# Kernel optimization log

Measured on AMD Instinct MI355X. Metric: run time of the kernel, lower is better.

The kernel has to match this reference:

```python
import jax, jax.numpy as jnp
import numpy as np

HIDDEN_DIM = 1024
N_EXPERTS = 4
EPS = 1e-6


def rmsnorm(x, w):
    return x * jax.lax.rsqrt(jnp.mean(x * x, axis=-1, keepdims=True) + EPS) * w


def setup_inputs() -> dict:
    key = jax.random.key(0)
    k1, k2, k3 = jax.random.split(key, 3)
    B, S = 16, 4096
    x = jax.random.normal(k1, (B, S, HIDDEN_DIM), dtype=jnp.float32)
    experts = jax.random.randint(k2, (B,), 0, N_EXPERTS)
    norm1_w = jnp.ones((HIDDEN_DIM,), dtype=jnp.float32)
    norm2_w = jnp.ones((HIDDEN_DIM,), dtype=jnp.float32)
    time_decay_logit = jnp.full((HIDDEN_DIM,), 2.0, dtype=jnp.float32)
    # stacked expert weights [n_experts, out, in] (torch Linear stores [out, in])
    W_experts = jax.random.normal(k3, (N_EXPERTS, HIDDEN_DIM, HIDDEN_DIM), dtype=jnp.float32) * 0.02
    return {"x": x, "experts": experts, "norm1_w": norm1_w,
            "time_decay_logit": time_decay_logit, "norm2_w": norm2_w,
            "W_experts": W_experts}


def reference(x, experts, norm1_w, time_decay_logit, norm2_w, W_experts):
    B, S, D = x.shape
    x_norm = rmsnorm(x, norm1_w)                      # [B,S,D]
    decay = jax.nn.sigmoid(time_decay_logit)          # [D]

    def step(state, x_t):
        state = state * decay + x_t * (1.0 - decay)
        return state, state

    init = jnp.zeros((B, D), dtype=x.dtype)
    _, states = jax.lax.scan(step, init, jnp.swapaxes(x_norm, 0, 1))  # [S,B,D]
    x = x + jnp.swapaxes(states, 0, 1)                # residual add

    pool_state = rmsnorm(x, norm2_w)[:, -1, :]        # [B,D]
    # gather each sample's expert weight and apply: y = relu(x @ W^T)
    W_b = W_experts[experts]                          # [B,out,in]
    out = jax.nn.relu(jnp.einsum('bd,bod->bo', pool_state, W_b))
    return out
```

## Files before the change

### kernel.cpp

```cpp
#include <hip/hip_runtime.h>
#include <math.h>

#define EPS 1e-6f
#define CH_L 64
#define TG 16

__global__ void k_prep(const float* __restrict__ logit, float* __restrict__ decay,
                       float* __restrict__ coef, int* __restrict__ Kp, int D, int S) {
    int tid = threadIdx.x;
    float local = 0.f;
    for (int d = tid; d < D; d += blockDim.x) {
        float dec = 1.f / (1.f + expf(-logit[d]));
        decay[d] = dec;
        coef[d]  = 1.f - dec;
        local = fmaxf(local, dec);
    }
    for (int off = 32; off; off >>= 1) local = fmaxf(local, __shfl_down(local, off));
    __shared__ float red[4];
    int wv = tid >> 6, ln = tid & 63;
    if (ln == 0) red[wv] = local;
    __syncthreads();
    if (tid == 0) {
        float maxd = fmaxf(fmaxf(red[0], red[1]), fmaxf(red[2], red[3]));
        float Kf;
        if (maxd <= 0.f) {
            Kf = 1.f;
        } else {
            float lg = logf(maxd);
            if (lg >= 0.f) Kf = (float)S;
            else           Kf = logf(1e-12f) / lg;
        }
        int K = (Kf >= (float)S) ? S : ((int)Kf + 1);
        *Kp = K;
    }
}

__global__ void k_rms(const float4* __restrict__ x4, const int* __restrict__ Kp,
                      float* __restrict__ inv_rms, int B, int S, int D, int nchunk) {
    int tg = blockIdx.x, b = blockIdx.y;
    int K = *Kp;
    int cmax = K / CH_L; if (cmax > nchunk - 1) cmax = nchunk - 1;
    int maxdist = (cmax + 1) * CH_L;
    int t0 = tg * TG;
    if (S - (t0 + TG) >= maxdist) return;
    int tid = threadIdx.x;
    int d4 = D >> 2;
    float s[TG];
#pragma unroll
    for (int i = 0; i < TG; i++) {
        float4 v = x4[((size_t)(b * S + t0 + i)) * d4 + tid];
        s[i] = v.x * v.x + v.y * v.y + v.z * v.z + v.w * v.w;
    }
#pragma unroll
    for (int i = 0; i < TG; i++)
        for (int off = 32; off; off >>= 1) s[i] += __shfl_down(s[i], off);
    __shared__ float red[4][TG];
    int wv = tid >> 6, ln = tid & 63;
    if (ln == 0) {
#pragma unroll
        for (int i = 0; i < TG; i++) red[wv][i] = s[i];
    }
    __syncthreads();
    if (tid < TG) {
        float tot = red[0][tid] + red[1][tid] + red[2][tid] + red[3][tid];
        inv_rms[(size_t)b * S + t0 + tid] = rsqrtf(tot / (float)D + EPS);
    }
}

__global__ void k_ema(const float4* __restrict__ x4, const float* __restrict__ inv_rms,
                      const float4* __restrict__ decay4, const float4* __restrict__ coef4,
                      const float4* __restrict__ w14, const int* __restrict__ Kp,
                      float4* __restrict__ partial4, int B, int S, int D, int nchunk) {
    int c = blockIdx.x, b = blockIdx.y;
    int K = *Kp;
    if (c * CH_L > K) return;
    int tid = threadIdx.x;
    int d4 = D >> 2;
    float4 dec = decay4[tid], cf = coef4[tid], w1 = w14[tid];
    float cx = cf.x * w1.x, cy = cf.y * w1.y, cz = cf.z * w1.z, cw = cf.w * w1.w;
    float4 acc = make_float4(0.f, 0.f, 0.f, 0.f);
    int t0 = S - (c + 1) * CH_L;
    const float4* xb = x4 + ((size_t)b * S + t0) * d4 + tid;
    const float* irp = inv_rms + (size_t)b * S + t0;
#pragma unroll 4
    for (int i = 0; i < CH_L; i++) {
        float ir = irp[i];
        float4 xv = xb[(size_t)i * d4];
        acc.x = acc.x * dec.x + xv.x * ir * cx;
        acc.y = acc.y * dec.y + xv.y * ir * cy;
        acc.z = acc.z * dec.z + xv.z * ir * cz;
        acc.w = acc.w * dec.w + xv.w * ir * cw;
    }
    partial4[((size_t)b * nchunk + c) * d4 + tid] = acc;
}

__global__ void k_pool(const float4* __restrict__ x4, const float4* __restrict__ partial4,
                       const float4* __restrict__ decay4, const float4* __restrict__ w24,
                       const int* __restrict__ Kp, float4* __restrict__ pool4,
                       int B, int S, int D, int nchunk) {
    int b = blockIdx.x;
    int tid = threadIdx.x;
    int K = *Kp;
    int cmax = K / CH_L; if (cmax > nchunk - 1) cmax = nchunk - 1;
    int d4 = D >> 2;
    float4 dec = decay4[tid];
    float4 st = make_float4(0.f, 0.f, 0.f, 0.f);
    for (int c = 0; c <= cmax; c++) {
        float4 p = partial4[((size_t)b * nchunk + c) * d4 + tid];
        float wx, wy, wz, ww;
        if (c == 0) { wx = wy = wz = ww = 1.f; }
        else {
            float e = (float)(c * CH_L);
            wx = powf(dec.x, e); wy = powf(dec.y, e);
            wz = powf(dec.z, e); ww = powf(dec.w, e);
        }
        st.x += p.x * wx; st.y += p.y * wy; st.z += p.z * wz; st.w += p.w * ww;
    }
    float4 xl = x4[((size_t)b * S + (S - 1)) * d4 + tid];
    float4 y = make_float4(xl.x + st.x, xl.y + st.y, xl.z + st.z, xl.w + st.w);
    float ss = y.x * y.x + y.y * y.y + y.z * y.z + y.w * y.w;
    for (int off = 32; off; off >>= 1) ss += __shfl_down(ss, off);
    __shared__ float red[4];
    __shared__ float tot;
    int wv = tid >> 6, ln = tid & 63;
    if (ln == 0) red[wv] = ss;
    __syncthreads();
    if (tid == 0) tot = red[0] + red[1] + red[2] + red[3];
    __syncthreads();
    float ir = rsqrtf(tot / (float)D + EPS);
    float4 w2 = w24[tid];
    float4 pl = make_float4(y.x * ir * w2.x, y.y * ir * w2.y,
                            y.z * ir * w2.z, y.w * ir * w2.w);
    pool4[(size_t)b * d4 + tid] = pl;
}

__global__ void k_matmul(const float* __restrict__ pool, const float* __restrict__ W,
                         const int* __restrict__ experts, float* __restrict__ out,
                         int B, int D, int O) {
    int b  = blockIdx.x;
    int og = blockIdx.y;
    int tid = threadIdx.x, wv = tid >> 6, ln = tid & 63;
    int o0 = og * 32 + wv * 8;
    int e = experts[b];
    const float4* pool4 = (const float4*)(pool + (size_t)b * D);
    float4 pv[4];
#pragma unroll
    for (int k = 0; k < 4; k++) pv[k] = pool4[k * 64 + ln];
#pragma unroll
    for (int j = 0; j < 8; j++) {
        const float4* Wr = (const float4*)(W + ((size_t)e * O + (o0 + j)) * D);
        float s = 0.f;
#pragma unroll
        for (int k = 0; k < 4; k++) {
            float4 w4 = Wr[k * 64 + ln];
            s += w4.x * pv[k].x + w4.y * pv[k].y + w4.z * pv[k].z + w4.w * pv[k].w;
        }
        for (int off = 32; off; off >>= 1) s += __shfl_down(s, off);
        if (ln == 0) out[(size_t)b * O + o0 + j] = fmaxf(s, 0.f);
    }
}

extern "C" void kernel_launch(void* const* d_in, const int* in_sizes, int n_in,
                              void* d_out, int out_size, void* d_ws, size_t ws_size,
                              hipStream_t stream) {
    const float* x       = (const float*)d_in[0];
    const int*   experts = (const int*)  d_in[1];
    const float* w1      = (const float*)d_in[2];
    const float* logit   = (const float*)d_in[3];
    const float* w2      = (const float*)d_in[4];
    const float* W       = (const float*)d_in[5];
    float* out = (float*)d_out;

    int B = in_sizes[1];
    int D = in_sizes[2];
    int S = in_sizes[0] / (B * D);
    int O = D;
    int nchunk = S / CH_L;

    float* ws      = (float*)d_ws;
    float* decay   = ws;
    float* coef    = ws + D;
    int*   Kp      = (int*)(ws + 2 * D);
    float* inv_rms = ws + 2 * D + 64;
    float* partial = inv_rms + (size_t)B * S;
    float* pool    = partial + (size_t)B * nchunk * D;

    k_prep<<<1, 256, 0, stream>>>(logit, decay, coef, Kp, D, S);
    k_rms<<<dim3(S / TG, B), 256, 0, stream>>>((const float4*)x, Kp, inv_rms,
                                               B, S, D, nchunk);
    k_ema<<<dim3(nchunk, B), 256, 0, stream>>>((const float4*)x, inv_rms,
                                               (const float4*)decay, (const float4*)coef,
                                               (const float4*)w1, Kp, (float4*)partial,
                                               B, S, D, nchunk);
    k_pool<<<B, 256, 0, stream>>>((const float4*)x, (const float4*)partial,
                                  (const float4*)decay, (const float4*)w2,
                                  Kp, (float4*)pool, B, S, D, nchunk);
    k_matmul<<<dim3(B, O / 32), 256, 0, stream>>>(pool, W, experts, out, B, D, O);
}
```

Before: 348.0 us.

## Fuse RMS norm into chunked EMA kernel with wave-parallel timesteps

Removes the separate per-timestep RMS kernel and computes each row's inverse RMS inside the EMA kernel via a wave-wide reduction. Each wave now handles interleaved timesteps with a decay^4 recurrence, and the four wave results are combined through shared memory. Chunk length drops to 16. The pool kernel replaces powf with a repeated multiplication by decay^16, and the prep kernel folds the norm weight into the coefficient. This cuts a launch and a pass over x, but adds smaller chunks and more partials for the pool loop.

```diff
diff --git a/kernel.cpp b/kernel.cpp
--- a/kernel.cpp
+++ b/kernel.cpp
@@ -2,141 +2,144 @@
 #include <math.h>
 
 #define EPS 1e-6f
-#define CH_L 64
-#define TG 16
+#define CH_L 16
 
-__global__ void k_prep(const float* __restrict__ logit, float* __restrict__ decay,
-                       float* __restrict__ coef, int* __restrict__ Kp, int D, int S) {
-    int tid = threadIdx.x;
-    float local = 0.f;
-    for (int d = tid; d < D; d += blockDim.x) {
-        float dec = 1.f / (1.f + expf(-logit[d]));
-        decay[d] = dec;
-        coef[d]  = 1.f - dec;
-        local = fmaxf(local, dec);
-    }
-    for (int off = 32; off; off >>= 1) local = fmaxf(local, __shfl_down(local, off));
+__global__ void k_prep(const float4* __restrict__ logit4, const float4* __restrict__ w14,
+                       float4* __restrict__ decay4, float4* __restrict__ cw4,
+                       int* __restrict__ Kp, int S) {
+    int tid = threadIdx.x, wv = tid >> 6, ln = tid & 63;
+    float4 lg = logit4[tid];
+    float4 w1 = w14[tid];
+    float4 dec;
+    dec.x = 1.f / (1.f + expf(-lg.x));
+    dec.y = 1.f / (1.f + expf(-lg.y));
+    dec.z = 1.f / (1.f + expf(-lg.z));
+    dec.w = 1.f / (1.f + expf(-lg.w));
+    decay4[tid] = dec;
+    float4 cw;
+    cw.x = (1.f - dec.x) * w1.x;
+    cw.y = (1.f - dec.y) * w1.y;
+    cw.z = (1.f - dec.z) * w1.z;
+    cw.w = (1.f - dec.w) * w1.w;
+    cw4[tid] = cw;
+    float m = fmaxf(fmaxf(dec.x, dec.y), fmaxf(dec.z, dec.w));
+    for (int off = 32; off; off >>= 1) m = fmaxf(m, __shfl_xor(m, off));
     __shared__ float red[4];
-    int wv = tid >> 6, ln = tid & 63;
-    if (ln == 0) red[wv] = local;
+    if (ln == 0) red[wv] = m;
     __syncthreads();
     if (tid == 0) {
         float maxd = fmaxf(fmaxf(red[0], red[1]), fmaxf(red[2], red[3]));
         float Kf;
-        if (maxd <= 0.f) {
-            Kf = 1.f;
-        } else {
-            float lg = logf(maxd);
-            if (lg >= 0.f) Kf = (float)S;
-            else           Kf = logf(1e-12f) / lg;
+        if (maxd <= 0.f) Kf = 1.f;
+        else {
+            float lgm = logf(maxd);
+            Kf = (lgm >= 0.f) ? (float)S : (logf(1e-12f) / lgm);
         }
         int K = (Kf >= (float)S) ? S : ((int)Kf + 1);
         *Kp = K;
     }
 }
 
-__global__ void k_rms(const float4* __restrict__ x4, const int* __restrict__ Kp,
-                      float* __restrict__ inv_rms, int B, int S, int D, int nchunk) {
-    int tg = blockIdx.x, b = blockIdx.y;
-    int K = *Kp;
-    int cmax = K / CH_L; if (cmax > nchunk - 1) cmax = nchunk - 1;
-    int maxdist = (cmax + 1) * CH_L;
-    int t0 = tg * TG;
-    if (S - (t0 + TG) >= maxdist) return;
-    int tid = threadIdx.x;
-    int d4 = D >> 2;
-    float s[TG];
+__global__ void k_ema(const float4* __restrict__ x4, const float4* __restrict__ decay4,
+                      const float4* __restrict__ cw4, const int* __restrict__ Kp,
+                      float4* __restrict__ partial4, int B, int S, int nchunk) {
+    int c = blockIdx.x, b = blockIdx.y;
+    if (c * CH_L > *Kp) return;
+    int tid = threadIdx.x, wv = tid >> 6, ln = tid & 63;
+
+    float4 dec[4], d4p[4], cwp[4];
 #pragma unroll
-    for (int i = 0; i < TG; i++) {
-        float4 v = x4[((size_t)(b * S + t0 + i)) * d4 + tid];
-        s[i] = v.x * v.x + v.y * v.y + v.z * v.z + v.w * v.w;
+    for (int k = 0; k < 4; k++) {
+        float4 d = decay4[k * 64 + ln];
+        float4 cw = cw4[k * 64 + ln];
+        float4 d2 = make_float4(d.x * d.x, d.y * d.y, d.z * d.z, d.w * d.w);
+        d4p[k] = make_float4(d2.x * d2.x, d2.y * d2.y, d2.z * d2.z, d2.w * d2.w);
+        float4 pw;
+        if (wv == 3)      pw = make_float4(1.f, 1.f, 1.f, 1.f);
+        else if (wv == 2) pw = d;
+        else if (wv == 1) pw = d2;
+        else              pw = make_float4(d2.x * d.x, d2.y * d.y, d2.z * d.z, d2.w * d.w);
+        cwp[k] = make_float4(cw.x * pw.x, cw.y * pw.y, cw.z * pw.z, cw.w * pw.w);
+        dec[k] = d;
     }
+
+    float4 acc[4];
 #pragma unroll
-    for (int i = 0; i < TG; i++)
-        for (int off = 32; off; off >>= 1) s[i] += __shfl_down(s[i], off);
-    __shared__ float red[4][TG];
-    int wv = tid >> 6, ln = tid & 63;
-    if (ln == 0) {
+    for (int k = 0; k < 4; k++) acc[k] = make_float4(0.f, 0.f, 0.f, 0.f);
+
+    int t0 = S - (c + 1) * CH_L;
 #pragma unroll
-        for (int i = 0; i < TG; i++) red[wv][i] = s[i];
+    for (int j = 0; j < 4; j++) {
+        int t = t0 + 4 * j + wv;
+        const float4* xp = x4 + ((size_t)b * S + t) * 256;
+        float4 xv[4];
+#pragma unroll
+        for (int k = 0; k < 4; k++) xv[k] = xp[k * 64 + ln];
+        float s = 0.f;
+#pragma unroll
+        for (int k = 0; k < 4; k++)
+            s += xv[k].x * xv[k].x + xv[k].y * xv[k].y + xv[k].z * xv[k].z + xv[k].w * xv[k].w;
+        for (int m = 1; m < 64; m <<= 1) s += __shfl_xor(s, m);
+        float ir = rsqrtf(s * (1.f / 1024.f) + EPS);
+#pragma unroll
+        for (int k = 0; k < 4; k++) {
+            acc[k].x = acc[k].x * d4p[k].x + xv[k].x * (cwp[k].x * ir);
+            acc[k].y = acc[k].y * d4p[k].y + xv[k].y * (cwp[k].y * ir);
+            acc[k].z = acc[k].z * d4p[k].z + xv[k].z * (cwp[k].z * ir);
+            acc[k].w = acc[k].w * d4p[k].w + xv[k].w * (cwp[k].w * ir);
+        }
     }
+
+    __shared__ float4 sm[4][256];
+#pragma unroll
+    for (int k = 0; k < 4; k++) sm[wv][k * 64 + ln] = acc[k];
     __syncthreads();
-    if (tid < TG) {
-        float tot = red[0][tid] + red[1][tid] + red[2][tid] + red[3][tid];
-        inv_rms[(size_t)b * S + t0 + tid] = rsqrtf(tot / (float)D + EPS);
-    }
-}
-
-__global__ void k_ema(const float4* __restrict__ x4, const float* __restrict__ inv_rms,
-                      const float4* __restrict__ decay4, const float4* __restrict__ coef4,
-                      const float4* __restrict__ w14, const int* __restrict__ Kp,
-                      float4* __restrict__ partial4, int B, int S, int D, int nchunk) {
-    int c = blockIdx.x, b = blockIdx.y;
-    int K = *Kp;
-    if (c * CH_L > K) return;
-    int tid = threadIdx.x;
-    int d4 = D >> 2;
-    float4 dec = decay4[tid], cf = coef4[tid], w1 = w14[tid];
-    float cx = cf.x * w1.x, cy = cf.y * w1.y, cz = cf.z * w1.z, cw = cf.w * w1.w;
-    float4 acc = make_float4(0.f, 0.f, 0.f, 0.f);
-    int t0 = S - (c + 1) * CH_L;
-    const float4* xb = x4 + ((size_t)b * S + t0) * d4 + tid;
-    const float* irp = inv_rms + (size_t)b * S + t0;
-#pragma unroll 4
-    for (int i = 0; i < CH_L; i++) {
-        float ir = irp[i];
-        float4 xv = xb[(size_t)i * d4];
-        acc.x = acc.x * dec.x + xv.x * ir * cx;
-        acc.y = acc.y * dec.y + xv.y * ir * cy;
-        acc.z = acc.z * dec.z + xv.z * ir * cz;
-        acc.w = acc.w * dec.w + xv.w * ir * cw;
-    }
-    partial4[((size_t)b * nchunk + c) * d4 + tid] = acc;
+    float4 r0 = sm[0][tid], r1 = sm[1][tid], r2 = sm[2][tid], r3 = sm[3][tid];
+    float4 r = make_float4(r0.x + r1.x + r2.x + r3.x, r0.y + r1.y + r2.y + r3.y,
+                           r0.z + r1.z + r2.z + r3.z, r0.w + r1.w + r2.w + r3.w);
+    partial4[((size_t)b * nchunk + c) * 256 + tid] = r;
 }
 
 __global__ void k_pool(const float4* __restrict__ x4, const float4* __restrict__ partial4,
                        const float4* __restrict__ decay4, const float4* __restrict__ w24,
                        const int* __restrict__ Kp, float4* __restrict__ pool4,
-                       int B, int S, int D, int nchunk) {
+                       int S, int nchunk) {
     int b = blockIdx.x;
-    int tid = threadIdx.x;
+    int tid = threadIdx.x, wv = tid >> 6, ln = tid & 63;
     int K = *Kp;
     int cmax = K / CH_L; if (cmax > nchunk - 1) cmax = nchunk - 1;
-    int d4 = D >> 2;
-    float4 dec = decay4[tid];
+    float4 d = decay4[tid];
+    float4 d2 = make_float4(d.x * d.x, d.y * d.y, d.z * d.z, d.w * d.w);
+    float4 d4 = make_float4(d2.x * d2.x, d2.y * d2.y, d2.z * d2.z, d2.w * d2.w);
+    float4 d8 = make_float4(d4.x * d4.x, d4.y * d4.y, d4.z * d4.z, d4.w * d4.w);
+    float4 dL = make_float4(d8.x * d8.x, d8.y * d8.y, d8.z * d8.z, d8.w * d8.w);
     float4 st = make_float4(0.f, 0.f, 0.f, 0.f);
+    float4 wgt = make_float4(1.f, 1.f, 1.f, 1.f);
     for (int c = 0; c <= cmax; c++) {
-        float4 p = partial4[((size_t)b * nchunk + c) * d4 + tid];
-        float wx, wy, wz, ww;
-        if (c == 0) { wx = wy = wz = ww = 1.f; }
-        else {
-            float e = (float)(c * CH_L);
-            wx = powf(dec.x, e); wy = powf(dec.y, e);
-            wz = powf(dec.z, e); ww = powf(dec.w, e);
-        }
-        st.x += p.x * wx; st.y += p.y * wy; st.z += p.z * wz; st.w += p.w * ww;
+        float4 p = partial4[((size_t)b * nchunk + c) * 256 + tid];
+        st.x += p.x * wgt.x; st.y += p.y * wgt.y;
+        st.z += p.z * wgt.z; st.w += p.w * wgt.w;
+        wgt.x *= dL.x; wgt.y *= dL.y; wgt.z *= dL.z; wgt.w *= dL.w;
     }
-    float4 xl = x4[((size_t)b * S + (S - 1)) * d4 + tid];
+    float4 xl = x4[((size_t)b * S + (S - 1)) * 256 + tid];
     float4 y = make_float4(xl.x + st.x, xl.y + st.y, xl.z + st.z, xl.w + st.w);
     float ss = y.x * y.x + y.y * y.y + y.z * y.z + y.w * y.w;
-    for (int off = 32; off; off >>= 1) ss += __shfl_down(ss, off);
+    for (int m = 1; m < 64; m <<= 1) ss += __shfl_xor(ss, m);
     __shared__ float red[4];
     __shared__ float tot;
-    int wv = tid >> 6, ln = tid & 63;
     if (ln == 0) red[wv] = ss;
     __syncthreads();
     if (tid == 0) tot = red[0] + red[1] + red[2] + red[3];
     __syncthreads();
-    float ir = rsqrtf(tot / (float)D + EPS);
+    float ir = rsqrtf(tot * (1.f / 1024.f) + EPS);
     float4 w2 = w24[tid];
-    float4 pl = make_float4(y.x * ir * w2.x, y.y * ir * w2.y,
-                            y.z * ir * w2.z, y.w * ir * w2.w);
-    pool4[(size_t)b * d4 + tid] = pl;
+    pool4[(size_t)b * 256 + tid] = make_float4(y.x * ir * w2.x, y.y * ir * w2.y,
+                                               y.z * ir * w2.z, y.w * ir * w2.w);
 }
 
 __global__ void k_matmul(const float* __restrict__ pool, const float* __restrict__ W,
                          const int* __restrict__ experts, float* __restrict__ out,
-                         int B, int D, int O) {
+                         int D, int O) {
     int b  = blockIdx.x;
     int og = blockIdx.y;
     int tid = threadIdx.x, wv = tid >> 6, ln = tid & 63;
@@ -179,21 +182,18 @@
 
     float* ws      = (float*)d_ws;
     float* decay   = ws;
-    float* coef    = ws + D;
+    float* cw      = ws + D;
     int*   Kp      = (int*)(ws + 2 * D);
-    float* inv_rms = ws + 2 * D + 64;
-    float* partial = inv_rms + (size_t)B * S;
+    float* partial = ws + 2 * D + 64;
     float* pool    = partial + (size_t)B * nchunk * D;
 
-    k_prep<<<1, 256, 0, stream>>>(logit, decay, coef, Kp, D, S);
-    k_rms<<<dim3(S / TG, B), 256, 0, stream>>>((const float4*)x, Kp, inv_rms,
-                                               B, S, D, nchunk);
-    k_ema<<<dim3(nchunk, B), 256, 0, stream>>>((const float4*)x, inv_rms,
-                                               (const float4*)decay, (const float4*)coef,
-                                               (const float4*)w1, Kp, (float4*)partial,
-                                               B, S, D, nchunk);
+    k_prep<<<1, 256, 0, stream>>>((const float4*)logit, (const float4*)w1,
+                                  (float4*)decay, (float4*)cw, Kp, S);
+    k_ema<<<dim3(nchunk, B), 256, 0, stream>>>((const float4*)x, (const float4*)decay,
+                                               (const float4*)cw, Kp,
+                                               (float4*)partial, B, S, nchunk);
     k_pool<<<B, 256, 0, stream>>>((const float4*)x, (const float4*)partial,
                                   (const float4*)decay, (const float4*)w2,
-                                  Kp, (float4*)pool, B, S, D, nchunk);
-    k_matmul<<<dim3(B, O / 32), 256, 0, stream>>>(pool, W, experts, out, B, D, O);
+                                  Kp, (float4*)pool, S, nchunk);
+    k_matmul<<<dim3(B, O / 32), 256, 0, stream>>>(pool, W, experts, out, D, O);
 }
```

Measured after the change: 331.7 us. 1.05x faster.
